# Kernel optimization log

Measured on AMD Instinct MI355X. Metric: run time of the kernel, lower is better.

Reference implementation:

```python
import jax, jax.numpy as jnp
import numpy as np

HEADS = 4
ATTN_DIM = 32
SCALE = ATTN_DIM ** -0.5
EPS = 1e-12  # F.normalize eps


def rmsnorm_chan(x, g):
    # x: (b, c, h, w); RMSNorm over channel dim: F.normalize(x, dim=1) * g * sqrt(c)
    c = x.shape[1]
    n = jnp.sqrt(jnp.sum(x * x, axis=1, keepdims=True))
    return x / jnp.maximum(n, EPS) * g[None, :, None, None] * jnp.sqrt(jnp.asarray(c, x.dtype))


def setup_inputs() -> dict:
    key = jax.random.key(0)
    ks = jax.random.split(key, 4)
    b, c, h, w = 16, 256, 64, 64
    hidden = HEADS * ATTN_DIM  # 128
    x = jax.random.normal(ks[0], (b, c, h, w), dtype=jnp.float32)
    norm_g = jnp.ones((c,), jnp.float32)
    w_qkv = jax.random.normal(ks[1], (3 * hidden, c), dtype=jnp.float32) * 0.02
    mem_kv = jax.random.normal(ks[2], (2, HEADS, ATTN_DIM, 4), dtype=jnp.float32)
    w_out = jax.random.normal(ks[3], (c, hidden), dtype=jnp.float32) * 0.02
    b_out = jnp.zeros((c,), jnp.float32)
    out_norm_g = jnp.ones((c,), jnp.float32)
    return {"x": x, "norm_g": norm_g, "w_qkv": w_qkv, "mem_kv": mem_kv,
            "w_out": w_out, "b_out": b_out, "out_norm_g": out_norm_g}


def reference(x, norm_g, w_qkv, mem_kv, w_out, b_out, out_norm_g):
    b, c, h, w = x.shape
    n = h * w
    xn = rmsnorm_chan(x, norm_g).reshape(b, c, n)  # pre-norm, flatten spatial
    # 1x1 conv (no bias) == channel matmul: (b, 3*hidden, n)
    qkv = jnp.einsum('oc,bcn->bon', w_qkv, xn)
    q, k, v = jnp.split(qkv, 3, axis=1)
    # (b, heads, d, n)
    q = q.reshape(b, HEADS, ATTN_DIM, n)
    k = k.reshape(b, HEADS, ATTN_DIM, n)
    v = v.reshape(b, HEADS, ATTN_DIM, n)
    # prepend memory kv (broadcast over batch): (b, heads, d, num_mem + n)
    mk = jnp.broadcast_to(mem_kv[0][None], (b, HEADS, ATTN_DIM, mem_kv.shape[-1]))
    mv = jnp.broadcast_to(mem_kv[1][None], (b, HEADS, ATTN_DIM, mem_kv.shape[-1]))
    k = jnp.concatenate([mk, k], axis=-1)
    v = jnp.concatenate([mv, v], axis=-1)
    q = jax.nn.softmax(q, axis=-2) * SCALE  # softmax over feature dim d
    k = jax.nn.softmax(k, axis=-1)          # softmax over token dim n
    context = jnp.einsum('bhdn,bhen->bhde', k, v)   # small d x e per head
    out = jnp.einsum('bhde,bhdn->bhen', context, q)  # (b, heads, e, n)
    out = out.reshape(b, HEADS * ATTN_DIM, h, w)
    # 1x1 conv with bias, then RMSNorm
    out = jnp.einsum('oc,bchw->bohw', w_out, out) + b_out[None, :, None, None]
    return rmsnorm_chan(out, out_norm_g)
```

## Files before the change

kernel.cpp:

```cpp
#include <hip/hip_runtime.h>
#include <hip/hip_bf16.h>

typedef __hip_bfloat16 bf16;
typedef __attribute__((ext_vector_type(8))) short bf16x8;
typedef __attribute__((ext_vector_type(4))) float floatx4;

#define NB 16
#define NC 256
#define NPIX 4096
#define NHID 128
#define NH 4
#define ND 32
#define NMEM 4
#define QSCALE 0.17677669529663687f

#define LGKM0()  asm volatile("s_waitcnt lgkmcnt(0)" ::: "memory")

__launch_bounds__(256)
__global__ void kW(const float* __restrict__ wqkv, const float* __restrict__ g,
                   bf16* __restrict__ wgpack, float* __restrict__ zbase){
  const int u = blockIdx.x*256 + threadIdx.x;
  for (int z = u; z < 65536 + 2048; z += 48*256) zbase[z] = 0.f;
  const int s = u / 1536;
  const int r = u - s*1536;
  const int tile = r >> 6, l = r & 63;
  const int row = tile*16 + (l & 15);
  const int kb  = s*32 + (l >> 4)*8;
  const float* wp = wqkv + (size_t)row*NC + kb;
  floatx4 w0 = *(const floatx4*)wp;
  floatx4 w1 = *(const floatx4*)(wp + 4);
  floatx4 g0 = *(const floatx4*)(g + kb);
  floatx4 g1 = *(const floatx4*)(g + kb + 4);
  alignas(16) bf16 tmp[8];
  #pragma unroll
  for (int i = 0; i < 4; ++i){
    tmp[i]   = __float2bfloat16(w0[i]*g0[i]);
    tmp[4+i] = __float2bfloat16(w1[i]*g1[i]);
  }
  *(uint4*)(wgpack + (size_t)u*8) = *(const uint4*)tmp;
}

__launch_bounds__(256)
__global__ void kA(const float* __restrict__ x, const bf16* __restrict__ wgpack,
                   float* __restrict__ dout,
                   float* __restrict__ ctxu, float* __restrict__ zacc){
  __shared__ char smem alignas(16) [48384];
  bf16 (*Pb)[72] = (bf16(*)[72])smem;
  bf16 (*Vb)[72] = (bf16(*)[72])(smem + 18432);
  float* ssqL = (float*)(smem + 47104);
  float* sL   = (float*)(smem + 48128);
  const int t = threadIdx.x;
  const int pb = blockIdx.x * 64, b = blockIdx.y;
  const int wv = t >> 6, lane = t & 63, m = lane & 15, q4 = lane >> 4;
  const int px_st = t & 63, cg_st = t >> 6;
  const float* xb = x + (size_t)b*NC*NPIX;
  float ssq = 0.f;
  float xr[2][8];
  bf16x8 af[2][6];

  auto xissue = [&](int c, float* dst){
    const float* xp = xb + (size_t)(c*32 + cg_st*8)*NPIX + pb + px_st;
    #pragma unroll
    for (int j = 0; j < 8; ++j) dst[j] = xp[(size_t)j*NPIX];
  };
  auto xwrite = [&](int c, const float* v){
    alignas(16) bf16 tmp[8];
    #pragma unroll
    for (int j = 0; j < 8; ++j){
      ssq += v[j]*v[j];
      tmp[j] = __float2bfloat16(v[j]);
    }
    bf16 (*Xb)[40] = (bf16(*)[40])(smem + 36864 + (c&1)*5120);
    *(uint4*)&Xb[px_st][cg_st*8] = *(const uint4*)tmp;
  };
  auto wload = [&](int c, int rt)->bf16x8 {
    return *(const bf16x8*)(wgpack + ((size_t)(c*24 + wv*6 + rt)*64 + lane)*8);
  };

  xissue(0, xr[0]);
  #pragma unroll
  for (int rt = 0; rt < 6; ++rt) af[0][rt] = wload(0, rt);
  xissue(1, xr[1]);
  xwrite(0, xr[0]);
  LGKM0();
  __builtin_amdgcn_s_barrier();

  floatx4 acc[6][4] = {};
  #pragma unroll
  for (int s = 0; s < 8; ++s){
    const int buf = s & 1;
    bf16 (*Xb)[40] = (bf16(*)[40])(smem + 36864 + buf*5120);
    bf16x8 bfr[4];
    #pragma unroll
    for (int pt = 0; pt < 4; ++pt)
      bfr[pt] = *(const bf16x8*)&Xb[pt*16 + m][q4*8];
    if (s < 7){
      #pragma unroll
      for (int rt = 0; rt < 6; ++rt) af[(s+1)&1][rt] = wload(s + 1, rt);
    }
    if (s < 6) xissue(s + 2, xr[buf]);
    #pragma unroll
    for (int rt = 0; rt < 6; ++rt)
      #pragma unroll
      for (int pt = 0; pt < 4; ++pt)
        acc[rt][pt] = __builtin_amdgcn_mfma_f32_16x16x32_bf16(af[buf][rt], bfr[pt], acc[rt][pt], 0, 0, 0);
    if (s < 7) xwrite(s + 1, xr[buf ^ 1]);
    LGKM0();
    __builtin_amdgcn_s_barrier();
  }
  ssqL[cg_st*64 + px_st] = ssq;
  __syncthreads();
  if (t < 64){
    float tot = ssqL[t] + ssqL[64 + t] + ssqL[128 + t] + ssqL[192 + t];
    sL[t] = 16.0f / fmaxf(sqrtf(tot), 1e-12f);
  }
  __syncthreads();
  float sv[4];
  #pragma unroll
  for (int pt = 0; pt < 4; ++pt) sv[pt] = sL[pt*16 + m];
  #pragma unroll
  for (int pr = 0; pr < 3; ++pr){
    const int ra = 2*pr, rb = 2*pr + 1;
    const int row0 = wv*96 + pr*32;
    const int type = row0 >> 7;
    if (type == 0){
      const int slice = row0 >> 5;
      const int j0 = (q4 & 1)*4;
      #pragma unroll
      for (int pt = 0; pt < 4; ++pt){
        float va[4], vb[4];
        float mx = -1e30f;
        #pragma unroll
        for (int r = 0; r < 4; ++r){
          va[r] = acc[ra][pt][r]*sv[pt];
          vb[r] = acc[rb][pt][r]*sv[pt];
          mx = fmaxf(mx, fmaxf(va[r], vb[r]));
        }
        mx = fmaxf(mx, __shfl_xor(mx, 16, 64));
        mx = fmaxf(mx, __shfl_xor(mx, 32, 64));
        float se = 0.f;
        #pragma unroll
        for (int r = 0; r < 4; ++r){
          va[r] = __expf(va[r] - mx); vb[r] = __expf(vb[r] - mx);
          se += va[r] + vb[r];
        }
        se += __shfl_xor(se, 16, 64);
        se += __shfl_xor(se, 32, 64);
        const float inv = QSCALE / se;
        alignas(8) bf16 pka[4], pkb[4];
        #pragma unroll
        for (int r = 0; r < 4; ++r){
          pka[r] = __float2bfloat16(va[r]*inv);
          pkb[r] = __float2bfloat16(vb[r]*inv);
        }
        const int ca = (slice*4 + pt)*4 + (q4 >> 1);
        const int cb = ca + 2;
        bf16* pa = (bf16*)(dout + (size_t)(b*NC + ca)*NPIX + pb) + m*8 + j0;
        bf16* pv = (bf16*)(dout + (size_t)(b*NC + cb)*NPIX + pb) + m*8 + j0;
        *(uint2*)pa = *(const uint2*)pka;
        *(uint2*)pv = *(const uint2*)pkb;
      }
    } else if (type == 1){
      const int d0 = row0 - 128;
      float za[4] = {}, zb[4] = {};
      #pragma unroll
      for (int pt = 0; pt < 4; ++pt){
        #pragma unroll
        for (int r = 0; r < 4; ++r){
          float pa = __expf(acc[ra][pt][r]*sv[pt]);
          float pv = __expf(acc[rb][pt][r]*sv[pt]);
          za[r] += pa; zb[r] += pv;
          Pb[d0      + q4*4 + r][pt*16 + m] = __float2bfloat16(pa);
          Pb[d0 + 16 + q4*4 + r][pt*16 + m] = __float2bfloat16(pv);
        }
      }
      #pragma unroll
      for (int r = 0; r < 4; ++r){
        #pragma unroll
        for (int o = 1; o < 16; o <<= 1){
          za[r] += __shfl_xor(za[r], o, 64);
          zb[r] += __shfl_xor(zb[r], o, 64);
        }
      }
      if (m == 0){
        #pragma unroll
        for (int r = 0; r < 4; ++r){
          atomicAdd(&zacc[b*NHID + d0      + q4*4 + r], za[r]);
          atomicAdd(&zacc[b*NHID + d0 + 16 + q4*4 + r], zb[r]);
        }
      }
    } else {
      const int v0 = row0 - 256;
      #pragma unroll
      for (int pt = 0; pt < 4; ++pt)
        #pragma unroll
        for (int r = 0; r < 4; ++r){
          Vb[v0      + q4*4 + r][pt*16 + m] = __float2bfloat16(acc[ra][pt][r]*sv[pt]);
          Vb[v0 + 16 + q4*4 + r][pt*16 + m] = __float2bfloat16(acc[rb][pt][r]*sv[pt]);
        }
    }
  }
  __syncthreads();
  floatx4 cx[2][2] = {};
  #pragma unroll
  for (int k0t = 0; k0t < 64; k0t += 32){
    bf16x8 af2[2], bf2[2];
    #pragma unroll
    for (int dt = 0; dt < 2; ++dt) af2[dt] = *(const bf16x8*)&Pb[wv*32 + dt*16 + m][k0t + q4*8];
    #pragma unroll
    for (int et = 0; et < 2; ++et) bf2[et] = *(const bf16x8*)&Vb[wv*32 + et*16 + m][k0t + q4*8];
    #pragma unroll
    for (int dt = 0; dt < 2; ++dt)
      #pragma unroll
      for (int et = 0; et < 2; ++et)
        cx[dt][et] = __builtin_amdgcn_mfma_f32_16x16x32_bf16(af2[dt], bf2[et], cx[dt][et], 0, 0, 0);
  }
  float* cb2 = ctxu + (size_t)(b*NH + wv)*ND*ND;
  #pragma unroll
  for (int dt = 0; dt < 2; ++dt)
    #pragma unroll
    for (int et = 0; et < 2; ++et)
      #pragma unroll
      for (int r = 0; r < 4; ++r)
        atomicAdd(&cb2[(dt*16 + q4*4 + r)*ND + et*16 + m], cx[dt][et][r]);
}

__launch_bounds__(256)
__global__ void k4_weff(const float* __restrict__ ctxu, const float* __restrict__ zacc,
                        const float* __restrict__ memkv, const float* __restrict__ wout,
                        bf16* __restrict__ wpack){
  __shared__ float ctxL[4][32][32];
  __shared__ float woutL[64][129];
  const int t = threadIdx.x;
  const int o0 = blockIdx.x * 64, b = blockIdx.y;
  {
    const float* ws = wout + (size_t)o0*NHID;
    #pragma unroll
    for (int i = 0; i < 32; ++i){
      const int idx = i*256 + t;
      woutL[idx >> 7][idx & 127] = ws[idx];
    }
  }
  if (t < 128){
    const int h = t >> 5;
    const float* mk = memkv + t*NMEM;
    float me[4]; float z = zacc[b*NHID + t];
    #pragma unroll
    for (int j = 0; j < 4; ++j){ me[j] = __expf(mk[j]); z += me[j]; }
    const float invz = 1.0f / z;
    const float* cp = ctxu + (size_t)(b*NH*ND + t)*ND;
    const float* mv = memkv + (size_t)(NHID + h*ND)*NMEM;
    #pragma unroll
    for (int e = 0; e < ND; ++e){
      float ce = cp[e];
      #pragma unroll
      for (int j = 0; j < 4; ++j) ce += me[j]*mv[e*NMEM + j];
      ctxL[h][t & 31][e] = ce * invz;
    }
  }
  __syncthreads();
  const int ol = t & 63, g = t >> 6;
  float out[32] = {};
  #pragma unroll
  for (int e = 0; e < 32; ++e){
    const float we = woutL[ol][g*32 + e];
    #pragma unroll
    for (int d = 0; d < 32; ++d) out[d] += ctxL[g][d][e] * we;
  }
  const int o = o0 + ol, tile = o >> 4, m16 = o & 15;
  #pragma unroll
  for (int q4k = 0; q4k < 4; ++q4k){
    alignas(16) bf16 tmp[8];
    #pragma unroll
    for (int j = 0; j < 8; ++j) tmp[j] = __float2bfloat16(out[q4k*8 + j]);
    *(uint4*)(wpack + ((size_t)((b*4 + g)*16 + tile)*64 + q4k*16 + m16)*8) = *(const uint4*)tmp;
  }
}

__launch_bounds__(256)
__global__ void k5_out(float* dout, const bf16* __restrict__ wpack,
                       const float* __restrict__ bout, const float* __restrict__ gout){
  __shared__ float red[256];
  __shared__ float nf[64];
  const int t = threadIdx.x;
  const int pb = blockIdx.x * 64, b = blockIdx.y;
  const int wv = t >> 6, lane = t & 63, m = lane & 15, q4 = lane >> 4;
  bf16x8 wf[4][4], qf[4][4];
  #pragma unroll
  for (int s = 0; s < 4; ++s){
    #pragma unroll
    for (int rt = 0; rt < 4; ++rt)
      wf[s][rt] = *(const bf16x8*)(wpack + ((size_t)((b*4 + s)*16 + wv*4 + rt)*64 + lane)*8);
    #pragma unroll
    for (int pt = 0; pt < 4; ++pt)
      qf[s][pt] = *(const bf16x8*)((const char*)(dout + (size_t)(b*NC + (s*4 + pt)*4 + q4)*NPIX + pb) + m*16);
  }
  floatx4 acc[4][4] = {};
  #pragma unroll
  for (int s = 0; s < 4; ++s)
    #pragma unroll
    for (int rt = 0; rt < 4; ++rt)
      #pragma unroll
      for (int pt = 0; pt < 4; ++pt)
        acc[rt][pt] = __builtin_amdgcn_mfma_f32_16x16x32_bf16(wf[s][rt], qf[s][pt], acc[rt][pt], 0, 0, 0);
  float ps[4] = {0.f, 0.f, 0.f, 0.f};
  #pragma unroll
  for (int rt = 0; rt < 4; ++rt){
    const int row = wv*64 + rt*16 + q4*4;
    #pragma unroll
    for (int r = 0; r < 4; ++r){
      const float bias = bout[row + r];
      #pragma unroll
      for (int pt = 0; pt < 4; ++pt){
        acc[rt][pt][r] += bias;
        ps[pt] += acc[rt][pt][r]*acc[rt][pt][r];
      }
    }
  }
  #pragma unroll
  for (int pt = 0; pt < 4; ++pt){
    ps[pt] += __shfl_xor(ps[pt], 16, 64);
    ps[pt] += __shfl_xor(ps[pt], 32, 64);
  }
  if (q4 == 0){
    #pragma unroll
    for (int pt = 0; pt < 4; ++pt) red[wv*64 + pt*16 + m] = ps[pt];
  }
  __syncthreads();
  if (t < 64){
    float tot = red[t] + red[64 + t] + red[128 + t] + red[192 + t];
    nf[t] = 16.0f / fmaxf(sqrtf(tot), 1e-12f);
  }
  __syncthreads();
  float nv[4];
  #pragma unroll
  for (int pt = 0; pt < 4; ++pt) nv[pt] = nf[pt*16 + m];
  #pragma unroll
  for (int rt = 0; rt < 4; ++rt){
    const int row = wv*64 + rt*16 + q4*4;
    #pragma unroll
    for (int r = 0; r < 4; ++r){
      const float gg = gout[row + r];
      float* op = dout + (size_t)(b*NC + row + r)*NPIX + pb + m;
      #pragma unroll
      for (int pt = 0; pt < 4; ++pt)
        op[pt*16] = acc[rt][pt][r]*nv[pt]*gg;
    }
  }
}

extern "C" void kernel_launch(void* const* d_in, const int* in_sizes, int n_in,
                              void* d_out, int out_size, void* d_ws, size_t ws_size,
                              hipStream_t stream) {
  (void)in_sizes; (void)n_in; (void)out_size; (void)ws_size;
  const float* x     = (const float*)d_in[0];
  const float* ng    = (const float*)d_in[1];
  const float* wqkv  = (const float*)d_in[2];
  const float* memkv = (const float*)d_in[3];
  const float* wout  = (const float*)d_in[4];
  const float* bout  = (const float*)d_in[5];
  const float* gout  = (const float*)d_in[6];
  float* dout = (float*)d_out;
  char* ws = (char*)d_ws;
  bf16*  wgpack = (bf16*)(ws);
  bf16*  wpack  = (bf16*)(ws + 196608);
  float* ctxu   = (float*)(ws + 1245184);
  float* zacc   = (float*)(ws + 1507328);

  kW     <<<dim3(48),      256, 0, stream>>>(wqkv, ng, wgpack, ctxu);
  kA     <<<dim3(64, 16),  256, 0, stream>>>(x, wgpack, dout, ctxu, zacc);
  k4_weff<<<dim3(4, 16),   256, 0, stream>>>(ctxu, zacc, memkv, wout, wpack);
  k5_out <<<dim3(64, 16),  256, 0, stream>>>(dout, wpack, bout, gout);
}
```

Measured before the change: 176.4 us.

## Process two pixel tiles per block and replace context atomics with partial slabs

Each kA block now loops over two 64-pixel sub-tiles, accumulating the per-head context in registers across both, and halves the grid. The context atomics are replaced by plain stores of per-block partial context slabs, which k4_weff then sums over 32 slabs per batch. This removes atomic contention on the small context buffer and the zeroing of that buffer, but halves the number of blocks in kA and adds a reduction read in k4_weff.

Measured after the change: 183.6 us. 1.04x slower.

```diff
diff --git a/kernel.cpp b/kernel.cpp
--- a/kernel.cpp
+++ b/kernel.cpp
@@ -18,9 +18,9 @@
 
 __launch_bounds__(256)
 __global__ void kW(const float* __restrict__ wqkv, const float* __restrict__ g,
-                   bf16* __restrict__ wgpack, float* __restrict__ zbase){
+                   bf16* __restrict__ wgpack, float* __restrict__ zacc){
   const int u = blockIdx.x*256 + threadIdx.x;
-  for (int z = u; z < 65536 + 2048; z += 48*256) zbase[z] = 0.f;
+  if (u < NB*NHID) zacc[u] = 0.f;
   const int s = u / 1536;
   const int r = u - s*1536;
   const int tile = r >> 6, l = r & 63;
@@ -43,190 +43,194 @@
 __launch_bounds__(256)
 __global__ void kA(const float* __restrict__ x, const bf16* __restrict__ wgpack,
                    float* __restrict__ dout,
-                   float* __restrict__ ctxu, float* __restrict__ zacc){
+                   float* __restrict__ ctxp, float* __restrict__ zacc){
   __shared__ char smem alignas(16) [48384];
   bf16 (*Pb)[72] = (bf16(*)[72])smem;
   bf16 (*Vb)[72] = (bf16(*)[72])(smem + 18432);
   float* ssqL = (float*)(smem + 47104);
   float* sL   = (float*)(smem + 48128);
   const int t = threadIdx.x;
-  const int pb = blockIdx.x * 64, b = blockIdx.y;
+  const int pxg = blockIdx.x, b = blockIdx.y;
   const int wv = t >> 6, lane = t & 63, m = lane & 15, q4 = lane >> 4;
   const int px_st = t & 63, cg_st = t >> 6;
   const float* xb = x + (size_t)b*NC*NPIX;
-  float ssq = 0.f;
   float xr[2][8];
   bf16x8 af[2][6];
-
-  auto xissue = [&](int c, float* dst){
-    const float* xp = xb + (size_t)(c*32 + cg_st*8)*NPIX + pb + px_st;
-    #pragma unroll
-    for (int j = 0; j < 8; ++j) dst[j] = xp[(size_t)j*NPIX];
-  };
-  auto xwrite = [&](int c, const float* v){
-    alignas(16) bf16 tmp[8];
-    #pragma unroll
-    for (int j = 0; j < 8; ++j){
-      ssq += v[j]*v[j];
-      tmp[j] = __float2bfloat16(v[j]);
-    }
-    bf16 (*Xb)[40] = (bf16(*)[40])(smem + 36864 + (c&1)*5120);
-    *(uint4*)&Xb[px_st][cg_st*8] = *(const uint4*)tmp;
-  };
-  auto wload = [&](int c, int rt)->bf16x8 {
-    return *(const bf16x8*)(wgpack + ((size_t)(c*24 + wv*6 + rt)*64 + lane)*8);
-  };
-
-  xissue(0, xr[0]);
-  #pragma unroll
-  for (int rt = 0; rt < 6; ++rt) af[0][rt] = wload(0, rt);
-  xissue(1, xr[1]);
-  xwrite(0, xr[0]);
-  LGKM0();
-  __builtin_amdgcn_s_barrier();
-
-  floatx4 acc[6][4] = {};
-  #pragma unroll
-  for (int s = 0; s < 8; ++s){
-    const int buf = s & 1;
-    bf16 (*Xb)[40] = (bf16(*)[40])(smem + 36864 + buf*5120);
-    bf16x8 bfr[4];
-    #pragma unroll
-    for (int pt = 0; pt < 4; ++pt)
-      bfr[pt] = *(const bf16x8*)&Xb[pt*16 + m][q4*8];
-    if (s < 7){
-      #pragma unroll
-      for (int rt = 0; rt < 6; ++rt) af[(s+1)&1][rt] = wload(s + 1, rt);
-    }
-    if (s < 6) xissue(s + 2, xr[buf]);
-    #pragma unroll
-    for (int rt = 0; rt < 6; ++rt)
-      #pragma unroll
-      for (int pt = 0; pt < 4; ++pt)
-        acc[rt][pt] = __builtin_amdgcn_mfma_f32_16x16x32_bf16(af[buf][rt], bfr[pt], acc[rt][pt], 0, 0, 0);
-    if (s < 7) xwrite(s + 1, xr[buf ^ 1]);
+  floatx4 cx[2][2] = {};
+
+  for (int sub = 0; sub < 2; ++sub){
+    const int pb = pxg*128 + sub*64;
+    float ssq = 0.f;
+
+    auto xissue = [&](int c, float* dst){
+      const float* xp = xb + (size_t)(c*32 + cg_st*8)*NPIX + pb + px_st;
+      #pragma unroll
+      for (int j = 0; j < 8; ++j) dst[j] = xp[(size_t)j*NPIX];
+    };
+    auto xwrite = [&](int c, const float* v){
+      alignas(16) bf16 tmp[8];
+      #pragma unroll
+      for (int j = 0; j < 8; ++j){
+        ssq += v[j]*v[j];
+        tmp[j] = __float2bfloat16(v[j]);
+      }
+      bf16 (*Xb)[40] = (bf16(*)[40])(smem + 36864 + (c&1)*5120);
+      *(uint4*)&Xb[px_st][cg_st*8] = *(const uint4*)tmp;
+    };
+    auto wload = [&](int c, int rt)->bf16x8 {
+      return *(const bf16x8*)(wgpack + ((size_t)(c*24 + wv*6 + rt)*64 + lane)*8);
+    };
+
+    xissue(0, xr[0]);
+    #pragma unroll
+    for (int rt = 0; rt < 6; ++rt) af[0][rt] = wload(0, rt);
+    xissue(1, xr[1]);
+    xwrite(0, xr[0]);
     LGKM0();
     __builtin_amdgcn_s_barrier();
-  }
-  ssqL[cg_st*64 + px_st] = ssq;
-  __syncthreads();
-  if (t < 64){
-    float tot = ssqL[t] + ssqL[64 + t] + ssqL[128 + t] + ssqL[192 + t];
-    sL[t] = 16.0f / fmaxf(sqrtf(tot), 1e-12f);
-  }
-  __syncthreads();
-  float sv[4];
-  #pragma unroll
-  for (int pt = 0; pt < 4; ++pt) sv[pt] = sL[pt*16 + m];
-  #pragma unroll
-  for (int pr = 0; pr < 3; ++pr){
-    const int ra = 2*pr, rb = 2*pr + 1;
-    const int row0 = wv*96 + pr*32;
-    const int type = row0 >> 7;
-    if (type == 0){
-      const int slice = row0 >> 5;
-      const int j0 = (q4 & 1)*4;
-      #pragma unroll
-      for (int pt = 0; pt < 4; ++pt){
-        float va[4], vb[4];
-        float mx = -1e30f;
+
+    floatx4 acc[6][4] = {};
+    #pragma unroll
+    for (int s = 0; s < 8; ++s){
+      const int buf = s & 1;
+      bf16 (*Xb)[40] = (bf16(*)[40])(smem + 36864 + buf*5120);
+      bf16x8 bfr[4];
+      #pragma unroll
+      for (int pt = 0; pt < 4; ++pt)
+        bfr[pt] = *(const bf16x8*)&Xb[pt*16 + m][q4*8];
+      if (s < 7){
+        #pragma unroll
+        for (int rt = 0; rt < 6; ++rt) af[(s+1)&1][rt] = wload(s + 1, rt);
+      }
+      if (s < 6) xissue(s + 2, xr[buf]);
+      #pragma unroll
+      for (int rt = 0; rt < 6; ++rt)
+        #pragma unroll
+        for (int pt = 0; pt < 4; ++pt)
+          acc[rt][pt] = __builtin_amdgcn_mfma_f32_16x16x32_bf16(af[buf][rt], bfr[pt], acc[rt][pt], 0, 0, 0);
+      if (s < 7) xwrite(s + 1, xr[buf ^ 1]);
+      LGKM0();
+      __builtin_amdgcn_s_barrier();
+    }
+    ssqL[cg_st*64 + px_st] = ssq;
+    __syncthreads();
+    if (t < 64){
+      float tot = ssqL[t] + ssqL[64 + t] + ssqL[128 + t] + ssqL[192 + t];
+      sL[t] = 16.0f / fmaxf(sqrtf(tot), 1e-12f);
+    }
+    __syncthreads();
+    float sv[4];
+    #pragma unroll
+    for (int pt = 0; pt < 4; ++pt) sv[pt] = sL[pt*16 + m];
+    #pragma unroll
+    for (int pr = 0; pr < 3; ++pr){
+      const int ra = 2*pr, rb = 2*pr + 1;
+      const int row0 = wv*96 + pr*32;
+      const int type = row0 >> 7;
+      if (type == 0){
+        const int slice = row0 >> 5;
+        const int j0 = (q4 & 1)*4;
+        #pragma unroll
+        for (int pt = 0; pt < 4; ++pt){
+          float va[4], vb[4];
+          float mx = -1e30f;
+          #pragma unroll
+          for (int r = 0; r < 4; ++r){
+            va[r] = acc[ra][pt][r]*sv[pt];
+            vb[r] = acc[rb][pt][r]*sv[pt];
+            mx = fmaxf(mx, fmaxf(va[r], vb[r]));
+          }
+          mx = fmaxf(mx, __shfl_xor(mx, 16, 64));
+          mx = fmaxf(mx, __shfl_xor(mx, 32, 64));
+          float se = 0.f;
+          #pragma unroll
+          for (int r = 0; r < 4; ++r){
+            va[r] = __expf(va[r] - mx); vb[r] = __expf(vb[r] - mx);
+            se += va[r] + vb[r];
+          }
+          se += __shfl_xor(se, 16, 64);
+          se += __shfl_xor(se, 32, 64);
+          const float inv = QSCALE / se;
+          alignas(8) bf16 pka[4], pkb[4];
+          #pragma unroll
+          for (int r = 0; r < 4; ++r){
+            pka[r] = __float2bfloat16(va[r]*inv);
+            pkb[r] = __float2bfloat16(vb[r]*inv);
+          }
+          const int ca = (slice*4 + pt)*4 + (q4 >> 1);
+          const int cb = ca + 2;
+          bf16* pa = (bf16*)(dout + (size_t)(b*NC + ca)*NPIX + pb) + m*8 + j0;
+          bf16* pv = (bf16*)(dout + (size_t)(b*NC + cb)*NPIX + pb) + m*8 + j0;
+          *(uint2*)pa = *(const uint2*)pka;
+          *(uint2*)pv = *(const uint2*)pkb;
+        }
+      } else if (type == 1){
+        const int d0 = row0 - 128;
+        float za[4] = {}, zb[4] = {};
+        #pragma unroll
+        for (int pt = 0; pt < 4; ++pt){
+          #pragma unroll
+          for (int r = 0; r < 4; ++r){
+            float pa = __expf(acc[ra][pt][r]*sv[pt]);
+            float pv = __expf(acc[rb][pt][r]*sv[pt]);
+            za[r] += pa; zb[r] += pv;
+            Pb[d0      + q4*4 + r][pt*16 + m] = __float2bfloat16(pa);
+            Pb[d0 + 16 + q4*4 + r][pt*16 + m] = __float2bfloat16(pv);
+          }
+        }
         #pragma unroll
         for (int r = 0; r < 4; ++r){
-          va[r] = acc[ra][pt][r]*sv[pt];
-          vb[r] = acc[rb][pt][r]*sv[pt];
-          mx = fmaxf(mx, fmaxf(va[r], vb[r]));
+          #pragma unroll
+          for (int o = 1; o < 16; o <<= 1){
+            za[r] += __shfl_xor(za[r], o, 64);
+            zb[r] += __shfl_xor(zb[r], o, 64);
+          }
         }
-        mx = fmaxf(mx, __shfl_xor(mx, 16, 64));
-        mx = fmaxf(mx, __shfl_xor(mx, 32, 64));
-        float se = 0.f;
-        #pragma unroll
-        for (int r = 0; r < 4; ++r){
-          va[r] = __expf(va[r] - mx); vb[r] = __expf(vb[r] - mx);
-          se += va[r] + vb[r];
+        if (m == 0){
+          #pragma unroll
+          for (int r = 0; r < 4; ++r){
+            atomicAdd(&zacc[b*NHID + d0      + q4*4 + r], za[r]);
+            atomicAdd(&zacc[b*NHID + d0 + 16 + q4*4 + r], zb[r]);
+          }
         }
-        se += __shfl_xor(se, 16, 64);
-        se += __shfl_xor(se, 32, 64);
-        const float inv = QSCALE / se;
-        alignas(8) bf16 pka[4], pkb[4];
-        #pragma unroll
-        for (int r = 0; r < 4; ++r){
-          pka[r] = __float2bfloat16(va[r]*inv);
-          pkb[r] = __float2bfloat16(vb[r]*inv);
-        }
-        const int ca = (slice*4 + pt)*4 + (q4 >> 1);
-        const int cb = ca + 2;
-        bf16* pa = (bf16*)(dout + (size_t)(b*NC + ca)*NPIX + pb) + m*8 + j0;
-        bf16* pv = (bf16*)(dout + (size_t)(b*NC + cb)*NPIX + pb) + m*8 + j0;
-        *(uint2*)pa = *(const uint2*)pka;
-        *(uint2*)pv = *(const uint2*)pkb;
+      } else {
+        const int v0 = row0 - 256;
+        #pragma unroll
+        for (int pt = 0; pt < 4; ++pt)
+          #pragma unroll
+          for (int r = 0; r < 4; ++r){
+            Vb[v0      + q4*4 + r][pt*16 + m] = __float2bfloat16(acc[ra][pt][r]*sv[pt]);
+            Vb[v0 + 16 + q4*4 + r][pt*16 + m] = __float2bfloat16(acc[rb][pt][r]*sv[pt]);
+          }
       }
-    } else if (type == 1){
-      const int d0 = row0 - 128;
-      float za[4] = {}, zb[4] = {};
-      #pragma unroll
-      for (int pt = 0; pt < 4; ++pt){
-        #pragma unroll
-        for (int r = 0; r < 4; ++r){
-          float pa = __expf(acc[ra][pt][r]*sv[pt]);
-          float pv = __expf(acc[rb][pt][r]*sv[pt]);
-          za[r] += pa; zb[r] += pv;
-          Pb[d0      + q4*4 + r][pt*16 + m] = __float2bfloat16(pa);
-          Pb[d0 + 16 + q4*4 + r][pt*16 + m] = __float2bfloat16(pv);
-        }
-      }
-      #pragma unroll
-      for (int r = 0; r < 4; ++r){
-        #pragma unroll
-        for (int o = 1; o < 16; o <<= 1){
-          za[r] += __shfl_xor(za[r], o, 64);
-          zb[r] += __shfl_xor(zb[r], o, 64);
-        }
-      }
-      if (m == 0){
-        #pragma unroll
-        for (int r = 0; r < 4; ++r){
-          atomicAdd(&zacc[b*NHID + d0      + q4*4 + r], za[r]);
-          atomicAdd(&zacc[b*NHID + d0 + 16 + q4*4 + r], zb[r]);
-        }
-      }
-    } else {
-      const int v0 = row0 - 256;
-      #pragma unroll
-      for (int pt = 0; pt < 4; ++pt)
-        #pragma unroll
-        for (int r = 0; r < 4; ++r){
-          Vb[v0      + q4*4 + r][pt*16 + m] = __float2bfloat16(acc[ra][pt][r]*sv[pt]);
-          Vb[v0 + 16 + q4*4 + r][pt*16 + m] = __float2bfloat16(acc[rb][pt][r]*sv[pt]);
-        }
-    }
-  }
-  __syncthreads();
-  floatx4 cx[2][2] = {};
-  #pragma unroll
-  for (int k0t = 0; k0t < 64; k0t += 32){
-    bf16x8 af2[2], bf2[2];
-    #pragma unroll
-    for (int dt = 0; dt < 2; ++dt) af2[dt] = *(const bf16x8*)&Pb[wv*32 + dt*16 + m][k0t + q4*8];
-    #pragma unroll
-    for (int et = 0; et < 2; ++et) bf2[et] = *(const bf16x8*)&Vb[wv*32 + et*16 + m][k0t + q4*8];
-    #pragma unroll
-    for (int dt = 0; dt < 2; ++dt)
-      #pragma unroll
-      for (int et = 0; et < 2; ++et)
-        cx[dt][et] = __builtin_amdgcn_mfma_f32_16x16x32_bf16(af2[dt], bf2[et], cx[dt][et], 0, 0, 0);
-  }
-  float* cb2 = ctxu + (size_t)(b*NH + wv)*ND*ND;
+    }
+    __syncthreads();
+    #pragma unroll
+    for (int k0t = 0; k0t < 64; k0t += 32){
+      bf16x8 af2[2], bf2[2];
+      #pragma unroll
+      for (int dt = 0; dt < 2; ++dt) af2[dt] = *(const bf16x8*)&Pb[wv*32 + dt*16 + m][k0t + q4*8];
+      #pragma unroll
+      for (int et = 0; et < 2; ++et) bf2[et] = *(const bf16x8*)&Vb[wv*32 + et*16 + m][k0t + q4*8];
+      #pragma unroll
+      for (int dt = 0; dt < 2; ++dt)
+        #pragma unroll
+        for (int et = 0; et < 2; ++et)
+          cx[dt][et] = __builtin_amdgcn_mfma_f32_16x16x32_bf16(af2[dt], bf2[et], cx[dt][et], 0, 0, 0);
+    }
+  }
+  float* cb2 = ctxp + (size_t)(b*32 + pxg)*4096 + wv*1024;
   #pragma unroll
   for (int dt = 0; dt < 2; ++dt)
     #pragma unroll
     for (int et = 0; et < 2; ++et)
       #pragma unroll
       for (int r = 0; r < 4; ++r)
-        atomicAdd(&cb2[(dt*16 + q4*4 + r)*ND + et*16 + m], cx[dt][et][r]);
+        cb2[(dt*16 + q4*4 + r)*32 + et*16 + m] = cx[dt][et][r];
 }
 
 __launch_bounds__(256)
-__global__ void k4_weff(const float* __restrict__ ctxu, const float* __restrict__ zacc,
+__global__ void k4_weff(const float* __restrict__ ctxp, const float* __restrict__ zacc,
                         const float* __restrict__ memkv, const float* __restrict__ wout,
                         bf16* __restrict__ wpack){
   __shared__ float ctxL[4][32][32];
@@ -241,21 +245,34 @@
       woutL[idx >> 7][idx & 127] = ws[idx];
     }
   }
+  {
+    floatx4 s4[4] = {};
+    for (int sb = 0; sb < 32; ++sb){
+      const float* slab = ctxp + (size_t)(b*32 + sb)*4096;
+      #pragma unroll
+      for (int i = 0; i < 4; ++i)
+        s4[i] += *(const floatx4*)(slab + i*1024 + t*4);
+    }
+    #pragma unroll
+    for (int i = 0; i < 4; ++i)
+      *(floatx4*)((float*)ctxL + i*1024 + t*4) = s4[i];
+  }
+  __syncthreads();
   if (t < 128){
-    const int h = t >> 5;
+    const int h = t >> 5, d = t & 31;
     const float* mk = memkv + t*NMEM;
     float me[4]; float z = zacc[b*NHID + t];
     #pragma unroll
     for (int j = 0; j < 4; ++j){ me[j] = __expf(mk[j]); z += me[j]; }
     const float invz = 1.0f / z;
-    const float* cp = ctxu + (size_t)(b*NH*ND + t)*ND;
+    float* cp = (float*)ctxL + h*1024 + d*32;
     const float* mv = memkv + (size_t)(NHID + h*ND)*NMEM;
     #pragma unroll
     for (int e = 0; e < ND; ++e){
       float ce = cp[e];
       #pragma unroll
       for (int j = 0; j < 4; ++j) ce += me[j]*mv[e*NMEM + j];
-      ctxL[h][t & 31][e] = ce * invz;
+      cp[e] = ce * invz;
     }
   }
   __syncthreads();
@@ -364,11 +381,11 @@
   char* ws = (char*)d_ws;
   bf16*  wgpack = (bf16*)(ws);
   bf16*  wpack  = (bf16*)(ws + 196608);
-  float* ctxu   = (float*)(ws + 1245184);
-  float* zacc   = (float*)(ws + 1507328);
-
-  kW     <<<dim3(48),      256, 0, stream>>>(wqkv, ng, wgpack, ctxu);
-  kA     <<<dim3(64, 16),  256, 0, stream>>>(x, wgpack, dout, ctxu, zacc);
-  k4_weff<<<dim3(4, 16),   256, 0, stream>>>(ctxu, zacc, memkv, wout, wpack);
+  float* zacc   = (float*)(ws + 1245184);
+  float* ctxp   = (float*)(ws + 1310720);
+
+  kW     <<<dim3(48),      256, 0, stream>>>(wqkv, ng, wgpack, zacc);
+  kA     <<<dim3(32, 16),  256, 0, stream>>>(x, wgpack, dout, ctxp, zacc);
+  k4_weff<<<dim3(4, 16),   256, 0, stream>>>(ctxp, zacc, memkv, wout, wpack);
   k5_out <<<dim3(64, 16),  256, 0, stream>>>(dout, wpack, bout, gout);
 }
```

## Shrink kA shared memory, roll main loop, and double-buffer k5 fragment loads

Applied to the files above, without the earlier changes.

In kA, the X staging buffers are moved to the start of shared memory so they alias the Pb region, which cuts the LDS footprint from about 48KB to 38KB and may allow more resident blocks. The 8-step main loop becomes a rolled loop with two manually unrolled halves, so buffer indices are compile-time constants while code size stays small. In k5_out, all 16 weight and 16 activation fragments are no longer loaded up front; they go through two rotating buffers, reducing register pressure. The risks are less latency hiding from fewer loads in flight and possible Pb/Xb aliasing hazards.

Measured after the change: 194.5 us. +10.2%, slower.

```diff
diff --git a/kernel.cpp b/kernel.cpp
--- a/kernel.cpp
+++ b/kernel.cpp
@@ -44,11 +44,11 @@
 __global__ void kA(const float* __restrict__ x, const bf16* __restrict__ wgpack,
                    float* __restrict__ dout,
                    float* __restrict__ ctxu, float* __restrict__ zacc){
-  __shared__ char smem alignas(16) [48384];
+  __shared__ char smem alignas(16) [38144];
   bf16 (*Pb)[72] = (bf16(*)[72])smem;
   bf16 (*Vb)[72] = (bf16(*)[72])(smem + 18432);
-  float* ssqL = (float*)(smem + 47104);
-  float* sL   = (float*)(smem + 48128);
+  float* ssqL = (float*)(smem + 36864);
+  float* sL   = (float*)(smem + 37888);
   const int t = threadIdx.x;
   const int pb = blockIdx.x * 64, b = blockIdx.y;
   const int wv = t >> 6, lane = t & 63, m = lane & 15, q4 = lane >> 4;
@@ -70,7 +70,7 @@
       ssq += v[j]*v[j];
       tmp[j] = __float2bfloat16(v[j]);
     }
-    bf16 (*Xb)[40] = (bf16(*)[40])(smem + 36864 + (c&1)*5120);
+    bf16 (*Xb)[40] = (bf16(*)[40])(smem + (c&1)*5120);
     *(uint4*)&Xb[px_st][cg_st*8] = *(const uint4*)tmp;
   };
   auto wload = [&](int c, int rt)->bf16x8 {
@@ -86,27 +86,46 @@
   __builtin_amdgcn_s_barrier();
 
   floatx4 acc[6][4] = {};
-  #pragma unroll
-  for (int s = 0; s < 8; ++s){
-    const int buf = s & 1;
-    bf16 (*Xb)[40] = (bf16(*)[40])(smem + 36864 + buf*5120);
-    bf16x8 bfr[4];
-    #pragma unroll
-    for (int pt = 0; pt < 4; ++pt)
-      bfr[pt] = *(const bf16x8*)&Xb[pt*16 + m][q4*8];
-    if (s < 7){
-      #pragma unroll
-      for (int rt = 0; rt < 6; ++rt) af[(s+1)&1][rt] = wload(s + 1, rt);
-    }
-    if (s < 6) xissue(s + 2, xr[buf]);
-    #pragma unroll
-    for (int rt = 0; rt < 6; ++rt)
-      #pragma unroll
-      for (int pt = 0; pt < 4; ++pt)
-        acc[rt][pt] = __builtin_amdgcn_mfma_f32_16x16x32_bf16(af[buf][rt], bfr[pt], acc[rt][pt], 0, 0, 0);
-    if (s < 7) xwrite(s + 1, xr[buf ^ 1]);
-    LGKM0();
-    __builtin_amdgcn_s_barrier();
+  #pragma unroll 1
+  for (int s2 = 0; s2 < 8; s2 += 2){
+    {
+      bf16 (*Xb)[40] = (bf16(*)[40])(smem + 0);
+      bf16x8 bfr[4];
+      #pragma unroll
+      for (int pt = 0; pt < 4; ++pt)
+        bfr[pt] = *(const bf16x8*)&Xb[pt*16 + m][q4*8];
+      #pragma unroll
+      for (int rt = 0; rt < 6; ++rt) af[1][rt] = wload(s2 + 1, rt);
+      if (s2 < 6) xissue(s2 + 2, xr[0]);
+      #pragma unroll
+      for (int rt = 0; rt < 6; ++rt)
+        #pragma unroll
+        for (int pt = 0; pt < 4; ++pt)
+          acc[rt][pt] = __builtin_amdgcn_mfma_f32_16x16x32_bf16(af[0][rt], bfr[pt], acc[rt][pt], 0, 0, 0);
+      xwrite(s2 + 1, xr[1]);
+      LGKM0();
+      __builtin_amdgcn_s_barrier();
+    }
+    {
+      bf16 (*Xb)[40] = (bf16(*)[40])(smem + 5120);
+      bf16x8 bfr[4];
+      #pragma unroll
+      for (int pt = 0; pt < 4; ++pt)
+        bfr[pt] = *(const bf16x8*)&Xb[pt*16 + m][q4*8];
+      if (s2 < 6){
+        #pragma unroll
+        for (int rt = 0; rt < 6; ++rt) af[0][rt] = wload(s2 + 2, rt);
+      }
+      if (s2 < 6) xissue(s2 + 3, xr[1]);
+      #pragma unroll
+      for (int rt = 0; rt < 6; ++rt)
+        #pragma unroll
+        for (int pt = 0; pt < 4; ++pt)
+          acc[rt][pt] = __builtin_amdgcn_mfma_f32_16x16x32_bf16(af[1][rt], bfr[pt], acc[rt][pt], 0, 0, 0);
+      if (s2 < 6) xwrite(s2 + 2, xr[0]);
+      LGKM0();
+      __builtin_amdgcn_s_barrier();
+    }
   }
   ssqL[cg_st*64 + px_st] = ssq;
   __syncthreads();
@@ -285,24 +304,30 @@
   const int t = threadIdx.x;
   const int pb = blockIdx.x * 64, b = blockIdx.y;
   const int wv = t >> 6, lane = t & 63, m = lane & 15, q4 = lane >> 4;
-  bf16x8 wf[4][4], qf[4][4];
+  bf16x8 wf[2][4], qf[2][4];
+  auto loadw = [&](int s, bf16x8* dst){
+    #pragma unroll
+    for (int rt = 0; rt < 4; ++rt)
+      dst[rt] = *(const bf16x8*)(wpack + ((size_t)((b*4 + s)*16 + wv*4 + rt)*64 + lane)*8);
+  };
+  auto loadq = [&](int s, bf16x8* dst){
+    #pragma unroll
+    for (int pt = 0; pt < 4; ++pt)
+      dst[pt] = *(const bf16x8*)((const char*)(dout + (size_t)(b*NC + (s*4 + pt)*4 + q4)*NPIX + pb) + m*16);
+  };
+  loadw(0, wf[0]); loadq(0, qf[0]);
+  loadw(1, wf[1]); loadq(1, qf[1]);
+  floatx4 acc[4][4] = {};
   #pragma unroll
   for (int s = 0; s < 4; ++s){
+    const int buf = s & 1;
     #pragma unroll
     for (int rt = 0; rt < 4; ++rt)
-      wf[s][rt] = *(const bf16x8*)(wpack + ((size_t)((b*4 + s)*16 + wv*4 + rt)*64 + lane)*8);
-    #pragma unroll
-    for (int pt = 0; pt < 4; ++pt)
-      qf[s][pt] = *(const bf16x8*)((const char*)(dout + (size_t)(b*NC + (s*4 + pt)*4 + q4)*NPIX + pb) + m*16);
-  }
-  floatx4 acc[4][4] = {};
-  #pragma unroll
-  for (int s = 0; s < 4; ++s)
-    #pragma unroll
-    for (int rt = 0; rt < 4; ++rt)
-      #pragma unroll
-      for (int pt = 0; pt < 4; ++pt)
-        acc[rt][pt] = __builtin_amdgcn_mfma_f32_16x16x32_bf16(wf[s][rt], qf[s][pt], acc[rt][pt], 0, 0, 0);
+      #pragma unroll
+      for (int pt = 0; pt < 4; ++pt)
+        acc[rt][pt] = __builtin_amdgcn_mfma_f32_16x16x32_bf16(wf[buf][rt], qf[buf][pt], acc[rt][pt], 0, 0, 0);
+    if (s < 2){ loadw(s + 2, wf[buf]); loadq(s + 2, qf[buf]); }
+  }
   float ps[4] = {0.f, 0.f, 0.f, 0.f};
   #pragma unroll
   for (int rt = 0; rt < 4; ++rt){
```

## Halve kA pixel tile to 32 for more blocks and double-buffer k5 operand loads

Applied to the files above, without the earlier changes.

kA now processes 32 pixels per block instead of 64 and launches twice as many blocks. This shrinks shared memory and accumulator registers so more blocks can be resident and the whole GPU is filled. The cost is twice as many atomics on the ctx and z accumulators, and the context MFMA has half the K depth per block. k5_out also switches from loading all four k-slices up front to a two-deep register double buffer, which lowers register pressure but may expose load latency.

Measured after the change: 199.1 us. +12.8%, slower.

```diff
diff --git a/kernel.cpp b/kernel.cpp
--- a/kernel.cpp
+++ b/kernel.cpp
@@ -13,8 +13,6 @@
 #define ND 32
 #define NMEM 4
 #define QSCALE 0.17677669529663687f
-
-#define LGKM0()  asm volatile("s_waitcnt lgkmcnt(0)" ::: "memory")
 
 __launch_bounds__(256)
 __global__ void kW(const float* __restrict__ wqkv, const float* __restrict__ g,
@@ -44,34 +42,36 @@
 __global__ void kA(const float* __restrict__ x, const bf16* __restrict__ wgpack,
                    float* __restrict__ dout,
                    float* __restrict__ ctxu, float* __restrict__ zacc){
-  __shared__ char smem alignas(16) [48384];
-  bf16 (*Pb)[72] = (bf16(*)[72])smem;
-  bf16 (*Vb)[72] = (bf16(*)[72])(smem + 18432);
-  float* ssqL = (float*)(smem + 47104);
-  float* sL   = (float*)(smem + 48128);
+  __shared__ char smem alignas(16) [21632];
+  bf16 (*Pb)[40] = (bf16(*)[40])smem;
+  bf16 (*Vb)[40] = (bf16(*)[40])(smem + 10240);
+  float* ssqL = (float*)(smem + 20480);
+  float* sL   = (float*)(smem + 21504);
   const int t = threadIdx.x;
-  const int pb = blockIdx.x * 64, b = blockIdx.y;
+  const int bx = blockIdx.x, b = blockIdx.y;
+  const int pb32 = bx * 32;
+  const int pb64 = (bx >> 1) * 64, hi = bx & 1;
   const int wv = t >> 6, lane = t & 63, m = lane & 15, q4 = lane >> 4;
-  const int px_st = t & 63, cg_st = t >> 6;
+  const int px_st = t & 31, cg_st = t >> 5;
   const float* xb = x + (size_t)b*NC*NPIX;
   float ssq = 0.f;
-  float xr[2][8];
+  float xr[2][4];
   bf16x8 af[2][6];
 
   auto xissue = [&](int c, float* dst){
-    const float* xp = xb + (size_t)(c*32 + cg_st*8)*NPIX + pb + px_st;
-    #pragma unroll
-    for (int j = 0; j < 8; ++j) dst[j] = xp[(size_t)j*NPIX];
+    const float* xp = xb + (size_t)(c*32 + cg_st*4)*NPIX + pb32 + px_st;
+    #pragma unroll
+    for (int j = 0; j < 4; ++j) dst[j] = xp[(size_t)j*NPIX];
   };
   auto xwrite = [&](int c, const float* v){
-    alignas(16) bf16 tmp[8];
-    #pragma unroll
-    for (int j = 0; j < 8; ++j){
+    alignas(8) bf16 tmp[4];
+    #pragma unroll
+    for (int j = 0; j < 4; ++j){
       ssq += v[j]*v[j];
       tmp[j] = __float2bfloat16(v[j]);
     }
-    bf16 (*Xb)[40] = (bf16(*)[40])(smem + 36864 + (c&1)*5120);
-    *(uint4*)&Xb[px_st][cg_st*8] = *(const uint4*)tmp;
+    bf16 (*Xb)[40] = (bf16(*)[40])(smem + (c&1)*2560);
+    *(uint2*)&Xb[px_st][cg_st*4] = *(const uint2*)tmp;
   };
   auto wload = [&](int c, int rt)->bf16x8 {
     return *(const bf16x8*)(wgpack + ((size_t)(c*24 + wv*6 + rt)*64 + lane)*8);
@@ -82,17 +82,16 @@
   for (int rt = 0; rt < 6; ++rt) af[0][rt] = wload(0, rt);
   xissue(1, xr[1]);
   xwrite(0, xr[0]);
-  LGKM0();
-  __builtin_amdgcn_s_barrier();
-
-  floatx4 acc[6][4] = {};
+  __syncthreads();
+
+  floatx4 acc[6][2] = {};
   #pragma unroll
   for (int s = 0; s < 8; ++s){
     const int buf = s & 1;
-    bf16 (*Xb)[40] = (bf16(*)[40])(smem + 36864 + buf*5120);
-    bf16x8 bfr[4];
-    #pragma unroll
-    for (int pt = 0; pt < 4; ++pt)
+    bf16 (*Xb)[40] = (bf16(*)[40])(smem + buf*2560);
+    bf16x8 bfr[2];
+    #pragma unroll
+    for (int pt = 0; pt < 2; ++pt)
       bfr[pt] = *(const bf16x8*)&Xb[pt*16 + m][q4*8];
     if (s < 7){
       #pragma unroll
@@ -102,22 +101,23 @@
     #pragma unroll
     for (int rt = 0; rt < 6; ++rt)
       #pragma unroll
-      for (int pt = 0; pt < 4; ++pt)
+      for (int pt = 0; pt < 2; ++pt)
         acc[rt][pt] = __builtin_amdgcn_mfma_f32_16x16x32_bf16(af[buf][rt], bfr[pt], acc[rt][pt], 0, 0, 0);
     if (s < 7) xwrite(s + 1, xr[buf ^ 1]);
-    LGKM0();
-    __builtin_amdgcn_s_barrier();
-  }
-  ssqL[cg_st*64 + px_st] = ssq;
-  __syncthreads();
-  if (t < 64){
-    float tot = ssqL[t] + ssqL[64 + t] + ssqL[128 + t] + ssqL[192 + t];
+    __syncthreads();
+  }
+  ssqL[cg_st*32 + px_st] = ssq;
+  __syncthreads();
+  if (t < 32){
+    float tot = 0.f;
+    #pragma unroll
+    for (int i = 0; i < 8; ++i) tot += ssqL[i*32 + t];
     sL[t] = 16.0f / fmaxf(sqrtf(tot), 1e-12f);
   }
   __syncthreads();
-  float sv[4];
-  #pragma unroll
-  for (int pt = 0; pt < 4; ++pt) sv[pt] = sL[pt*16 + m];
+  float sv[2];
+  #pragma unroll
+  for (int pt = 0; pt < 2; ++pt) sv[pt] = sL[pt*16 + m];
   #pragma unroll
   for (int pr = 0; pr < 3; ++pr){
     const int ra = 2*pr, rb = 2*pr + 1;
@@ -127,7 +127,7 @@
       const int slice = row0 >> 5;
       const int j0 = (q4 & 1)*4;
       #pragma unroll
-      for (int pt = 0; pt < 4; ++pt){
+      for (int pt = 0; pt < 2; ++pt){
         float va[4], vb[4];
         float mx = -1e30f;
         #pragma unroll
@@ -153,10 +153,10 @@
           pka[r] = __float2bfloat16(va[r]*inv);
           pkb[r] = __float2bfloat16(vb[r]*inv);
         }
-        const int ca = (slice*4 + pt)*4 + (q4 >> 1);
+        const int ca = (slice*4 + (hi*2 + pt))*4 + (q4 >> 1);
         const int cb = ca + 2;
-        bf16* pa = (bf16*)(dout + (size_t)(b*NC + ca)*NPIX + pb) + m*8 + j0;
-        bf16* pv = (bf16*)(dout + (size_t)(b*NC + cb)*NPIX + pb) + m*8 + j0;
+        bf16* pa = (bf16*)(dout + (size_t)(b*NC + ca)*NPIX + pb64) + m*8 + j0;
+        bf16* pv = (bf16*)(dout + (size_t)(b*NC + cb)*NPIX + pb64) + m*8 + j0;
         *(uint2*)pa = *(const uint2*)pka;
         *(uint2*)pv = *(const uint2*)pkb;
       }
@@ -164,7 +164,7 @@
       const int d0 = row0 - 128;
       float za[4] = {}, zb[4] = {};
       #pragma unroll
-      for (int pt = 0; pt < 4; ++pt){
+      for (int pt = 0; pt < 2; ++pt){
         #pragma unroll
         for (int r = 0; r < 4; ++r){
           float pa = __expf(acc[ra][pt][r]*sv[pt]);
@@ -192,7 +192,7 @@
     } else {
       const int v0 = row0 - 256;
       #pragma unroll
-      for (int pt = 0; pt < 4; ++pt)
+      for (int pt = 0; pt < 2; ++pt)
         #pragma unroll
         for (int r = 0; r < 4; ++r){
           Vb[v0      + q4*4 + r][pt*16 + m] = __float2bfloat16(acc[ra][pt][r]*sv[pt]);
@@ -202,13 +202,12 @@
   }
   __syncthreads();
   floatx4 cx[2][2] = {};
-  #pragma unroll
-  for (int k0t = 0; k0t < 64; k0t += 32){
+  {
     bf16x8 af2[2], bf2[2];
     #pragma unroll
-    for (int dt = 0; dt < 2; ++dt) af2[dt] = *(const bf16x8*)&Pb[wv*32 + dt*16 + m][k0t + q4*8];
-    #pragma unroll
-    for (int et = 0; et < 2; ++et) bf2[et] = *(const bf16x8*)&Vb[wv*32 + et*16 + m][k0t + q4*8];
+    for (int dt = 0; dt < 2; ++dt) af2[dt] = *(const bf16x8*)&Pb[wv*32 + dt*16 + m][q4*8];
+    #pragma unroll
+    for (int et = 0; et < 2; ++et) bf2[et] = *(const bf16x8*)&Vb[wv*32 + et*16 + m][q4*8];
     #pragma unroll
     for (int dt = 0; dt < 2; ++dt)
       #pragma unroll
@@ -285,24 +284,30 @@
   const int t = threadIdx.x;
   const int pb = blockIdx.x * 64, b = blockIdx.y;
   const int wv = t >> 6, lane = t & 63, m = lane & 15, q4 = lane >> 4;
-  bf16x8 wf[4][4], qf[4][4];
+  bf16x8 wf[2][4], qf[2][4];
+  auto loadw = [&](int s, bf16x8* dst){
+    #pragma unroll
+    for (int rt = 0; rt < 4; ++rt)
+      dst[rt] = *(const bf16x8*)(wpack + ((size_t)((b*4 + s)*16 + wv*4 + rt)*64 + lane)*8);
+  };
+  auto loadq = [&](int s, bf16x8* dst){
+    #pragma unroll
+    for (int pt = 0; pt < 4; ++pt)
+      dst[pt] = *(const bf16x8*)((const char*)(dout + (size_t)(b*NC + (s*4 + pt)*4 + q4)*NPIX + pb) + m*16);
+  };
+  loadw(0, wf[0]); loadq(0, qf[0]);
+  loadw(1, wf[1]); loadq(1, qf[1]);
+  floatx4 acc[4][4] = {};
   #pragma unroll
   for (int s = 0; s < 4; ++s){
+    const int buf = s & 1;
     #pragma unroll
     for (int rt = 0; rt < 4; ++rt)
-      wf[s][rt] = *(const bf16x8*)(wpack + ((size_t)((b*4 + s)*16 + wv*4 + rt)*64 + lane)*8);
-    #pragma unroll
-    for (int pt = 0; pt < 4; ++pt)
-      qf[s][pt] = *(const bf16x8*)((const char*)(dout + (size_t)(b*NC + (s*4 + pt)*4 + q4)*NPIX + pb) + m*16);
-  }
-  floatx4 acc[4][4] = {};
-  #pragma unroll
-  for (int s = 0; s < 4; ++s)
-    #pragma unroll
-    for (int rt = 0; rt < 4; ++rt)
       #pragma unroll
       for (int pt = 0; pt < 4; ++pt)
-        acc[rt][pt] = __builtin_amdgcn_mfma_f32_16x16x32_bf16(wf[s][rt], qf[s][pt], acc[rt][pt], 0, 0, 0);
+        acc[rt][pt] = __builtin_amdgcn_mfma_f32_16x16x32_bf16(wf[buf][rt], qf[buf][pt], acc[rt][pt], 0, 0, 0);
+    if (s < 2){ loadw(s + 2, wf[buf]); loadq(s + 2, qf[buf]); }
+  }
   float ps[4] = {0.f, 0.f, 0.f, 0.f};
   #pragma unroll
   for (int rt = 0; rt < 4; ++rt){
@@ -368,7 +373,7 @@
   float* zacc   = (float*)(ws + 1507328);
 
   kW     <<<dim3(48),      256, 0, stream>>>(wqkv, ng, wgpack, ctxu);
-  kA     <<<dim3(64, 16),  256, 0, stream>>>(x, wgpack, dout, ctxu, zacc);
+  kA     <<<dim3(128, 16), 256, 0, stream>>>(x, wgpack, dout, ctxu, zacc);
   k4_weff<<<dim3(4, 16),   256, 0, stream>>>(ctxu, zacc, memkv, wout, wpack);
   k5_out <<<dim3(64, 16),  256, 0, stream>>>(dout, wpack, bout, gout);
 }
```
